# Kernel optimization log

Measured on AMD Instinct MI355X. Metric: run time of the kernel, lower is better.

The kernel has to match this reference:

```python
import jax, jax.numpy as jnp
import numpy as np

N_NODES = 50000
N_EDGES = 1600000
N_FEATURES = 1433
HIDDEN = 256
N_CLASSES = 7


def setup_inputs() -> dict:
    key = jax.random.key(0)
    ks = jax.random.split(key, 5)
    x = jax.random.normal(ks[0], (N_NODES, N_FEATURES), dtype=jnp.float32)
    edge_index = jax.random.randint(ks[1], (2, N_EDGES), 0, N_NODES, dtype=jnp.int64)
    # Glorot-style init like PyG's Linear inside GCNConv
    W1 = jax.random.normal(ks[2], (N_FEATURES, HIDDEN), dtype=jnp.float32) * (1.0 / np.sqrt(N_FEATURES))
    b1 = jnp.zeros((HIDDEN,), dtype=jnp.float32)
    W2 = jax.random.normal(ks[3], (HIDDEN, N_CLASSES), dtype=jnp.float32) * (1.0 / np.sqrt(HIDDEN))
    b2 = jnp.zeros((N_CLASSES,), dtype=jnp.float32)
    return {"x": x, "edge_index": edge_index, "W1": W1, "b1": b1, "W2": W2, "b2": b2}


def _gcn_conv(x, W, b, src, dst, n_nodes):
    """PyG GCNConv: add self-loops, symmetric deg^{-1/2} norm, linear, scatter-add, +bias."""
    h = x @ W  # [N, out]
    loop = jnp.arange(n_nodes, dtype=src.dtype)
    src2 = jnp.concatenate([src, loop])
    dst2 = jnp.concatenate([dst, loop])
    ones = jnp.ones(src2.shape[0], dtype=h.dtype)
    deg = jax.ops.segment_sum(ones, dst2, num_segments=n_nodes)
    dinv = jnp.where(deg > 0, jax.lax.rsqrt(deg), 0.0)
    norm = dinv[src2] * dinv[dst2]  # [E+N]
    msg = h[src2] * norm[:, None]   # gather + scale
    out = jax.ops.segment_sum(msg, dst2, num_segments=n_nodes)
    return out + b


def reference(x, edge_index, W1, b1, W2, b2):
    src, dst = edge_index[0], edge_index[1]
    h = _gcn_conv(x, W1, b1, src, dst, N_NODES)
    h = jax.nn.relu(h)
    # dropout p=0.5 is identity in eval mode (training=False)
    out = _gcn_conv(h, W2, b2, src, dst, N_NODES)
    return out
```

## Files before the change

kernel.cpp:

```cpp
#include <hip/hip_runtime.h>
#include <hip/hip_bf16.h>


#define N_NODES_   50000
#define NB_ROWS_   50048
#define N_EDGES_   1600000
#define N_FEAT_    1433
#define K_PAD_     1440
#define HIDDEN_    256
#define N_CLASSES_ 7

typedef __attribute__((ext_vector_type(8))) short short8;
typedef __attribute__((ext_vector_type(4))) float f32x4;
typedef unsigned int u32;
typedef unsigned short u16;

__device__ __forceinline__ u16 f2bf(float f) {
    __hip_bfloat16 h = __float2bfloat16(f);
    return *(u16*)&h;
}
__device__ __forceinline__ float bf2f(u16 u) {
    return __uint_as_float((u32)u << 16);
}
__device__ __forceinline__ void global_to_lds16(const void* g, void* l) {
    __builtin_amdgcn_global_load_lds(
        (const __attribute__((address_space(1))) u32*)g,
        (__attribute__((address_space(3))) u32*)l, 16, 0, 0);
}

__global__ void deg_kernel(const int* __restrict__ dst, int* __restrict__ deg) {
    int i = blockIdx.x * blockDim.x + threadIdx.x;
    if (i < N_EDGES_) atomicAdd(&deg[dst[i]], 1);
}

__global__ void dinv_kernel(const int* __restrict__ deg, float* __restrict__ dinv) {
    int i = blockIdx.x * blockDim.x + threadIdx.x;
    if (i < N_NODES_) dinv[i] = rsqrtf((float)(deg[i] + 1));
}

#define SCAN_T 256
#define CHUNK_ ((N_NODES_ + SCAN_T - 1) / SCAN_T)
__global__ __launch_bounds__(SCAN_T) void scan_kernel(const int* __restrict__ deg,
                                                      int* __restrict__ row_ptr,
                                                      int* __restrict__ cursor) {
    __shared__ int sums[SCAN_T];
    int t = threadIdx.x;
    int lo = t * CHUNK_, hi = min(lo + CHUNK_, N_NODES_);
    int s = 0;
    for (int i = lo; i < hi; i++) s += deg[i];
    sums[t] = s;
    __syncthreads();
    for (int off = 1; off < SCAN_T; off <<= 1) {
        int v = (t >= off) ? sums[t - off] : 0;
        __syncthreads();
        sums[t] += v;
        __syncthreads();
    }
    int run = (t == 0) ? 0 : sums[t - 1];
    for (int i = lo; i < hi; i++) {
        row_ptr[i] = run;
        cursor[i]  = run;
        run += deg[i];
    }
    if (t == SCAN_T - 1) row_ptr[N_NODES_] = run;
}

__global__ void csr_scatter_kernel(const int* __restrict__ src, const int* __restrict__ dst,
                                   int* __restrict__ cursor, int* __restrict__ csr_src) {
    int i = blockIdx.x * blockDim.x + threadIdx.x;
    if (i >= N_EDGES_) return;
    int d = dst[i];
    int pos = atomicAdd(&cursor[d], 1);
    csr_src[pos] = src[i];
}

__global__ __launch_bounds__(256) void cvt_kernel(const float* __restrict__ x,
                                                  u16* __restrict__ xb) {
    int row = blockIdx.x;
    int t = threadIdx.x;
    const float* xr = x + (long)row * N_FEAT_;
    u16* xbr = xb + (long)row * K_PAD_;
    bool valid = row < N_NODES_;
    for (int k = t; k < K_PAD_; k += 256) {
        float v = (valid && k < N_FEAT_) ? xr[k] : 0.f;
        xbr[k] = f2bf(v);
    }
}

__global__ void w1t_kernel(const float* __restrict__ W1, u16* __restrict__ W1T) {
    int gid = blockIdx.x * blockDim.x + threadIdx.x;
    if (gid >= HIDDEN_ * K_PAD_) return;
    int k = gid % K_PAD_, n = gid / K_PAD_;
    float v = (k < N_FEAT_) ? W1[(long)k * HIDDEN_ + n] : 0.f;
    W1T[(long)n * K_PAD_ + k] = f2bf(v);
}

#define BM 128
#define BN 128
#define BK 32
__global__ __launch_bounds__(256) void gemm1_mfma(const u16* __restrict__ A,
                                                  const u16* __restrict__ BT,
                                                  u16* __restrict__ C) {
    __shared__ u16 As[BM * BK];
    __shared__ u16 Bs[BN * BK];

    const int tid  = threadIdx.x;
    const int lane = tid & 63;
    const int wv   = tid >> 6;
    const int row0 = blockIdx.x * BM;
    const int col0 = blockIdx.y * BN;
    const int wr0  = (wv >> 1) * 64;
    const int wc0  = (wv & 1) * 64;

    f32x4 acc[4][4] = {};

    const int srow = lane >> 2;
    const int skk  = (lane & 3) * 8;

    for (int k0 = 0; k0 < K_PAD_; k0 += BK) {
        #pragma unroll
        for (int j = 0; j < 2; j++) {
            int rbase = wv * 32 + j * 16;
            const u16* g = A + (long)(row0 + rbase + srow) * K_PAD_ + k0 + skk;
            global_to_lds16(g, &As[rbase * BK]);
        }
        #pragma unroll
        for (int j = 0; j < 2; j++) {
            int rbase = j * 64 + wv * 16;
            const u16* g = BT + (long)(col0 + rbase + srow) * K_PAD_ + k0 + skk;
            global_to_lds16(g, &Bs[rbase * BK]);
        }
        __syncthreads();

        const int fm = lane & 15;
        const int fq = (lane >> 4) * 8;
        short8 af[4], bf[4];
        #pragma unroll
        for (int mi = 0; mi < 4; mi++)
            af[mi] = *(const short8*)&As[(wr0 + mi * 16 + fm) * BK + fq];
        #pragma unroll
        for (int ni = 0; ni < 4; ni++)
            bf[ni] = *(const short8*)&Bs[(wc0 + ni * 16 + fm) * BK + fq];
        #pragma unroll
        for (int mi = 0; mi < 4; mi++)
            #pragma unroll
            for (int ni = 0; ni < 4; ni++)
                acc[mi][ni] = __builtin_amdgcn_mfma_f32_16x16x32_bf16(af[mi], bf[ni], acc[mi][ni], 0, 0, 0);
        __syncthreads();
    }

    const int fm = lane & 15;
    const int q4 = (lane >> 4) * 4;
    #pragma unroll
    for (int mi = 0; mi < 4; mi++) {
        #pragma unroll
        for (int r = 0; r < 4; r++) {
            int gm = row0 + wr0 + mi * 16 + q4 + r;
            if (gm < N_NODES_) {
                #pragma unroll
                for (int ni = 0; ni < 4; ni++) {
                    int gn = col0 + wc0 + ni * 16 + fm;
                    C[(long)gm * HIDDEN_ + gn] = f2bf(acc[mi][ni][r]);
                }
            }
        }
    }
}

__global__ __launch_bounds__(256) void agg_gemm2_kernel(const u16* __restrict__ h1b,
                                                        const int* __restrict__ row_ptr,
                                                        const int* __restrict__ csr_src,
                                                        const float* __restrict__ dinv,
                                                        const float* __restrict__ b1,
                                                        const float* __restrict__ W2,
                                                        float* __restrict__ h2) {
    __shared__ float w2s[HIDDEN_ * N_CLASSES_];
    __shared__ float b1s[HIDDEN_];
    int tid = threadIdx.x;
    for (int i = tid; i < HIDDEN_ * N_CLASSES_; i += 256) w2s[i] = W2[i];
    for (int i = tid; i < HIDDEN_; i += 256) b1s[i] = b1[i];
    __syncthreads();

    int wave = tid >> 6;
    int lane = tid & 63;
    int node = blockIdx.x * 4 + wave;
    if (node >= N_NODES_) return;

    int e0 = row_ptr[node], e1 = row_ptr[node + 1];
    float ax = 0.f, ay = 0.f, az = 0.f, aw = 0.f;
    for (int base = e0; base < e1; base += 64) {
        int myE = base + lane;
        int sL = 0;
        float nsL = 0.f;
        if (myE < e1) {
            sL = csr_src[myE];
            nsL = dinv[sL];
        }
        int cnt4 = (min(64, e1 - base) + 3) & ~3;
        for (int j = 0; j < cnt4; j += 4) {
            #pragma unroll
            for (int t = 0; t < 4; t++) {
                int s   = __shfl(sL, j + t, 64);
                float ns = __shfl(nsL, j + t, 64);
                ushort4 u = ((const ushort4*)(h1b + (long)s * HIDDEN_))[lane];
                ax += bf2f(u.x) * ns;
                ay += bf2f(u.y) * ns;
                az += bf2f(u.z) * ns;
                aw += bf2f(u.w) * ns;
            }
        }
    }
    float nd = dinv[node];
    ushort4 su = ((const ushort4*)(h1b + (long)node * HIDDEN_))[lane];
    float xv[4];
    xv[0] = fmaxf(ax * nd + bf2f(su.x) * nd * nd + b1s[lane * 4 + 0], 0.f);
    xv[1] = fmaxf(ay * nd + bf2f(su.y) * nd * nd + b1s[lane * 4 + 1], 0.f);
    xv[2] = fmaxf(az * nd + bf2f(su.z) * nd * nd + b1s[lane * 4 + 2], 0.f);
    xv[3] = fmaxf(aw * nd + bf2f(su.w) * nd * nd + b1s[lane * 4 + 3], 0.f);

    float p[N_CLASSES_];
    #pragma unroll
    for (int c = 0; c < N_CLASSES_; c++) {
        float a = 0.f;
        #pragma unroll
        for (int i = 0; i < 4; i++)
            a += xv[i] * w2s[(lane * 4 + i) * N_CLASSES_ + c];
        p[c] = a;
    }
    #pragma unroll
    for (int off = 32; off > 0; off >>= 1)
        #pragma unroll
        for (int c = 0; c < N_CLASSES_; c++)
            p[c] += __shfl_down(p[c], off, 64);
    if (lane == 0) {
        #pragma unroll
        for (int c = 0; c < N_CLASSES_; c++)
            h2[(long)node * N_CLASSES_ + c] = p[c];
    }
}

__global__ void out_kernel(const float* __restrict__ h2,
                           const int* __restrict__ row_ptr,
                           const int* __restrict__ csr_src,
                           const float* __restrict__ dinv,
                           const float* __restrict__ b2,
                           float* __restrict__ out) {
    long gid = (long)blockIdx.x * blockDim.x + threadIdx.x;
    int node = (int)(gid >> 3);
    int c = (int)(gid & 7);
    if (node >= N_NODES_ || c >= N_CLASSES_) return;
    int e0 = row_ptr[node], e1 = row_ptr[node + 1];
    float acc = 0.f;
    for (int e = e0; e < e1; e++) {
        int s = csr_src[e];
        acc += h2[(long)s * N_CLASSES_ + c] * dinv[s];
    }
    float nd = dinv[node];
    out[(long)node * N_CLASSES_ + c] =
        acc * nd + h2[(long)node * N_CLASSES_ + c] * nd * nd + b2[c];
}

extern "C" void kernel_launch(void* const* d_in, const int* in_sizes, int n_in,
                              void* d_out, int out_size, void* d_ws, size_t ws_size,
                              hipStream_t stream) {
    const float* x   = (const float*)d_in[0];
    const int*   ei  = (const int*)d_in[1];
    const int*   src = ei;
    const int*   dst = ei + N_EDGES_;
    const float* W1  = (const float*)d_in[2];
    const float* b1  = (const float*)d_in[3];
    const float* W2  = (const float*)d_in[4];
    const float* b2  = (const float*)d_in[5];
    float* out = (float*)d_out;

    char* ws = (char*)d_ws;
    size_t off = 0;
    auto alloc = [&](size_t bytes) { void* p = ws + off; off = (off + bytes + 255) & ~(size_t)255; return p; };
    u16*   xb      = (u16*)alloc((size_t)NB_ROWS_ * K_PAD_ * 2);
    u16*   h1b     = (u16*)alloc((size_t)N_NODES_ * HIDDEN_ * 2);
    u16*   w1t     = (u16*)alloc((size_t)HIDDEN_ * K_PAD_ * 2);
    float* h2      = (float*)alloc((size_t)N_NODES_ * N_CLASSES_ * 4);
    int*   deg     = (int*)alloc((size_t)N_NODES_ * 4);
    float* dinv    = (float*)alloc((size_t)N_NODES_ * 4);
    int*   row_ptr = (int*)alloc((size_t)(N_NODES_ + 1) * 4);
    int*   cursor  = (int*)alloc((size_t)N_NODES_ * 4);
    int*   csr_src = (int*)alloc((size_t)N_EDGES_ * 4);

    hipMemsetAsync(deg, 0, (size_t)N_NODES_ * 4, stream);

    deg_kernel<<<(N_EDGES_ + 255) / 256, 256, 0, stream>>>(dst, deg);
    dinv_kernel<<<(N_NODES_ + 255) / 256, 256, 0, stream>>>(deg, dinv);
    scan_kernel<<<1, SCAN_T, 0, stream>>>(deg, row_ptr, cursor);
    csr_scatter_kernel<<<(N_EDGES_ + 255) / 256, 256, 0, stream>>>(src, dst, cursor, csr_src);

    cvt_kernel<<<NB_ROWS_, 256, 0, stream>>>(x, xb);
    w1t_kernel<<<(HIDDEN_ * K_PAD_ + 255) / 256, 256, 0, stream>>>(W1, w1t);

    gemm1_mfma<<<dim3(NB_ROWS_ / BM, HIDDEN_ / BN), 256, 0, stream>>>(xb, w1t, h1b);

    agg_gemm2_kernel<<<(N_NODES_ + 3) / 4, 256, 0, stream>>>(h1b, row_ptr, csr_src, dinv, b1, W2, h2);

    long out_threads = (long)N_NODES_ * 8;
    out_kernel<<<(unsigned)((out_threads + 255) / 256), 256, 0, stream>>>(h2, row_ptr, csr_src, dinv, b2, out);
}
```

Baseline: 964.3 us.

## Prescale features by source dinv, parallelize CSR scan, vectorize conversion and gathers

Folds the source-side deg^-1/2 factor into the GEMM1 epilogue and the layer-2 projection, so the gather loops no longer load dinv per edge. Zero-padded sentinel rows let unrolled gathers skip bounds handling. The single-block scan becomes a three-kernel multi-block scan, the bf16 conversion writes 8-wide vectors, and the next edge-index batch is prefetched in aggregation. This adds extra launches and memsets and changes the h2 row stride to 8.

After: 893.8 us. 1.08x faster.

```diff
diff --git a/kernel.cpp b/kernel.cpp
--- a/kernel.cpp
+++ b/kernel.cpp
@@ -9,8 +9,10 @@
 #define K_PAD_     1440
 #define HIDDEN_    256
 #define N_CLASSES_ 7
+#define NPART_     ((N_NODES_ + 255) / 256)
 
 typedef __attribute__((ext_vector_type(8))) short short8;
+typedef __attribute__((ext_vector_type(8))) unsigned short ushort8;
 typedef __attribute__((ext_vector_type(4))) float f32x4;
 typedef unsigned int u32;
 typedef unsigned short u16;
@@ -38,31 +40,59 @@
     if (i < N_NODES_) dinv[i] = rsqrtf((float)(deg[i] + 1));
 }
 
-#define SCAN_T 256
-#define CHUNK_ ((N_NODES_ + SCAN_T - 1) / SCAN_T)
-__global__ __launch_bounds__(SCAN_T) void scan_kernel(const int* __restrict__ deg,
-                                                      int* __restrict__ row_ptr,
-                                                      int* __restrict__ cursor) {
-    __shared__ int sums[SCAN_T];
+__global__ __launch_bounds__(256) void scan1_kernel(const int* __restrict__ deg,
+                                                    int* __restrict__ partial) {
+    __shared__ int ws[4];
+    int t = threadIdx.x, b = blockIdx.x;
+    int idx = b * 256 + t;
+    int v = (idx < N_NODES_) ? deg[idx] : 0;
+    #pragma unroll
+    for (int off = 32; off > 0; off >>= 1) v += __shfl_down(v, off, 64);
+    if ((t & 63) == 0) ws[t >> 6] = v;
+    __syncthreads();
+    if (t == 0) partial[b] = ws[0] + ws[1] + ws[2] + ws[3];
+}
+
+__global__ __launch_bounds__(256) void scan2_kernel(int* __restrict__ partial,
+                                                    int* __restrict__ blk_off) {
+    __shared__ int sh[256];
     int t = threadIdx.x;
-    int lo = t * CHUNK_, hi = min(lo + CHUNK_, N_NODES_);
-    int s = 0;
-    for (int i = lo; i < hi; i++) s += deg[i];
-    sums[t] = s;
+    int v = (t < NPART_) ? partial[t] : 0;
+    sh[t] = v;
     __syncthreads();
-    for (int off = 1; off < SCAN_T; off <<= 1) {
-        int v = (t >= off) ? sums[t - off] : 0;
-        __syncthreads();
-        sums[t] += v;
-        __syncthreads();
-    }
-    int run = (t == 0) ? 0 : sums[t - 1];
-    for (int i = lo; i < hi; i++) {
-        row_ptr[i] = run;
-        cursor[i]  = run;
-        run += deg[i];
-    }
-    if (t == SCAN_T - 1) row_ptr[N_NODES_] = run;
+    #pragma unroll
+    for (int off = 1; off < 256; off <<= 1) {
+        int a = (t >= off) ? sh[t - off] : 0;
+        __syncthreads();
+        sh[t] += a;
+        __syncthreads();
+    }
+    if (t < NPART_) blk_off[t] = sh[t] - v;
+}
+
+__global__ __launch_bounds__(256) void scan3_kernel(const int* __restrict__ deg,
+                                                    const int* __restrict__ blk_off,
+                                                    int* __restrict__ row_ptr,
+                                                    int* __restrict__ cursor) {
+    __shared__ int sh[256];
+    int t = threadIdx.x, b = blockIdx.x;
+    int idx = b * 256 + t;
+    int v = (idx < N_NODES_) ? deg[idx] : 0;
+    sh[t] = v;
+    __syncthreads();
+    #pragma unroll
+    for (int off = 1; off < 256; off <<= 1) {
+        int a = (t >= off) ? sh[t - off] : 0;
+        __syncthreads();
+        sh[t] += a;
+        __syncthreads();
+    }
+    if (idx < N_NODES_) {
+        int rp = blk_off[b] + sh[t] - v;
+        row_ptr[idx] = rp;
+        cursor[idx]  = rp;
+    }
+    if (idx == 0) row_ptr[N_NODES_] = N_EDGES_;
 }
 
 __global__ void csr_scatter_kernel(const int* __restrict__ src, const int* __restrict__ dst,
@@ -74,17 +104,22 @@
     csr_src[pos] = src[i];
 }
 
-__global__ __launch_bounds__(256) void cvt_kernel(const float* __restrict__ x,
+__global__ __launch_bounds__(192) void cvt_kernel(const float* __restrict__ x,
                                                   u16* __restrict__ xb) {
     int row = blockIdx.x;
     int t = threadIdx.x;
+    if (t >= K_PAD_ / 8) return;
+    int k0 = t * 8;
     const float* xr = x + (long)row * N_FEAT_;
-    u16* xbr = xb + (long)row * K_PAD_;
-    bool valid = row < N_NODES_;
-    for (int k = t; k < K_PAD_; k += 256) {
-        float v = (valid && k < N_FEAT_) ? xr[k] : 0.f;
-        xbr[k] = f2bf(v);
-    }
+    bool vrow = row < N_NODES_;
+    ushort8 o;
+    #pragma unroll
+    for (int j = 0; j < 8; j++) {
+        int k = k0 + j;
+        float v = (vrow && k < N_FEAT_) ? xr[k] : 0.f;
+        o[j] = f2bf(v);
+    }
+    *(ushort8*)(xb + (long)row * K_PAD_ + k0) = o;
 }
 
 __global__ void w1t_kernel(const float* __restrict__ W1, u16* __restrict__ W1T) {
@@ -100,6 +135,7 @@
 #define BK 32
 __global__ __launch_bounds__(256) void gemm1_mfma(const u16* __restrict__ A,
                                                   const u16* __restrict__ BT,
+                                                  const float* __restrict__ dinv,
                                                   u16* __restrict__ C) {
     __shared__ u16 As[BM * BK];
     __shared__ u16 Bs[BN * BK];
@@ -157,23 +193,24 @@
         for (int r = 0; r < 4; r++) {
             int gm = row0 + wr0 + mi * 16 + q4 + r;
             if (gm < N_NODES_) {
+                float sc = dinv[gm];
                 #pragma unroll
                 for (int ni = 0; ni < 4; ni++) {
                     int gn = col0 + wc0 + ni * 16 + fm;
-                    C[(long)gm * HIDDEN_ + gn] = f2bf(acc[mi][ni][r]);
+                    C[(long)gm * HIDDEN_ + gn] = f2bf(acc[mi][ni][r] * sc);
                 }
             }
         }
     }
 }
 
-__global__ __launch_bounds__(256) void agg_gemm2_kernel(const u16* __restrict__ h1b,
+__global__ __launch_bounds__(256) void agg_gemm2_kernel(const u16* __restrict__ h1s,
                                                         const int* __restrict__ row_ptr,
                                                         const int* __restrict__ csr_src,
                                                         const float* __restrict__ dinv,
                                                         const float* __restrict__ b1,
                                                         const float* __restrict__ W2,
-                                                        float* __restrict__ h2) {
+                                                        float* __restrict__ h2s) {
     __shared__ float w2s[HIDDEN_ * N_CLASSES_];
     __shared__ float b1s[HIDDEN_];
     int tid = threadIdx.x;
@@ -188,35 +225,32 @@
 
     int e0 = row_ptr[node], e1 = row_ptr[node + 1];
     float ax = 0.f, ay = 0.f, az = 0.f, aw = 0.f;
+
+    int sL = (e0 + lane < e1) ? csr_src[e0 + lane] : N_NODES_;
     for (int base = e0; base < e1; base += 64) {
-        int myE = base + lane;
-        int sL = 0;
-        float nsL = 0.f;
-        if (myE < e1) {
-            sL = csr_src[myE];
-            nsL = dinv[sL];
-        }
-        int cnt4 = (min(64, e1 - base) + 3) & ~3;
-        for (int j = 0; j < cnt4; j += 4) {
+        int sCur = sL;
+        int nb = base + 64;
+        if (nb < e1) sL = (nb + lane < e1) ? csr_src[nb + lane] : N_NODES_;
+        int cnt8 = (min(64, e1 - base) + 7) & ~7;
+        for (int j = 0; j < cnt8; j += 8) {
             #pragma unroll
-            for (int t = 0; t < 4; t++) {
-                int s   = __shfl(sL, j + t, 64);
-                float ns = __shfl(nsL, j + t, 64);
-                ushort4 u = ((const ushort4*)(h1b + (long)s * HIDDEN_))[lane];
-                ax += bf2f(u.x) * ns;
-                ay += bf2f(u.y) * ns;
-                az += bf2f(u.z) * ns;
-                aw += bf2f(u.w) * ns;
+            for (int t = 0; t < 8; t++) {
+                int s = __shfl(sCur, j + t, 64);
+                ushort4 u = ((const ushort4*)(h1s + (long)s * HIDDEN_))[lane];
+                ax += bf2f(u.x);
+                ay += bf2f(u.y);
+                az += bf2f(u.z);
+                aw += bf2f(u.w);
             }
         }
     }
     float nd = dinv[node];
-    ushort4 su = ((const ushort4*)(h1b + (long)node * HIDDEN_))[lane];
+    ushort4 su = ((const ushort4*)(h1s + (long)node * HIDDEN_))[lane];
     float xv[4];
-    xv[0] = fmaxf(ax * nd + bf2f(su.x) * nd * nd + b1s[lane * 4 + 0], 0.f);
-    xv[1] = fmaxf(ay * nd + bf2f(su.y) * nd * nd + b1s[lane * 4 + 1], 0.f);
-    xv[2] = fmaxf(az * nd + bf2f(su.z) * nd * nd + b1s[lane * 4 + 2], 0.f);
-    xv[3] = fmaxf(aw * nd + bf2f(su.w) * nd * nd + b1s[lane * 4 + 3], 0.f);
+    xv[0] = fmaxf((ax + bf2f(su.x)) * nd + b1s[lane * 4 + 0], 0.f);
+    xv[1] = fmaxf((ay + bf2f(su.y)) * nd + b1s[lane * 4 + 1], 0.f);
+    xv[2] = fmaxf((az + bf2f(su.z)) * nd + b1s[lane * 4 + 2], 0.f);
+    xv[3] = fmaxf((aw + bf2f(su.w)) * nd + b1s[lane * 4 + 3], 0.f);
 
     float p[N_CLASSES_];
     #pragma unroll
@@ -235,11 +269,11 @@
     if (lane == 0) {
         #pragma unroll
         for (int c = 0; c < N_CLASSES_; c++)
-            h2[(long)node * N_CLASSES_ + c] = p[c];
-    }
-}
-
-__global__ void out_kernel(const float* __restrict__ h2,
+            h2s[(long)node * 8 + c] = p[c] * nd;
+    }
+}
+
+__global__ void out_kernel(const float* __restrict__ h2s,
                            const int* __restrict__ row_ptr,
                            const int* __restrict__ csr_src,
                            const float* __restrict__ dinv,
@@ -251,13 +285,20 @@
     if (node >= N_NODES_ || c >= N_CLASSES_) return;
     int e0 = row_ptr[node], e1 = row_ptr[node + 1];
     float acc = 0.f;
-    for (int e = e0; e < e1; e++) {
-        int s = csr_src[e];
-        acc += h2[(long)s * N_CLASSES_ + c] * dinv[s];
+    for (int e = e0; e < e1; e += 4) {
+        int s0 = csr_src[e];
+        int s1 = (e + 1 < e1) ? csr_src[e + 1] : N_NODES_;
+        int s2 = (e + 2 < e1) ? csr_src[e + 2] : N_NODES_;
+        int s3 = (e + 3 < e1) ? csr_src[e + 3] : N_NODES_;
+        float v0 = h2s[(long)s0 * 8 + c];
+        float v1 = h2s[(long)s1 * 8 + c];
+        float v2 = h2s[(long)s2 * 8 + c];
+        float v3 = h2s[(long)s3 * 8 + c];
+        acc += (v0 + v1) + (v2 + v3);
     }
     float nd = dinv[node];
     out[(long)node * N_CLASSES_ + c] =
-        acc * nd + h2[(long)node * N_CLASSES_ + c] * nd * nd + b2[c];
+        (acc + h2s[(long)node * 8 + c]) * nd + b2[c];
 }
 
 extern "C" void kernel_launch(void* const* d_in, const int* in_sizes, int n_in,
@@ -277,29 +318,35 @@
     size_t off = 0;
     auto alloc = [&](size_t bytes) { void* p = ws + off; off = (off + bytes + 255) & ~(size_t)255; return p; };
     u16*   xb      = (u16*)alloc((size_t)NB_ROWS_ * K_PAD_ * 2);
-    u16*   h1b     = (u16*)alloc((size_t)N_NODES_ * HIDDEN_ * 2);
+    u16*   h1s     = (u16*)alloc((size_t)(N_NODES_ + 1) * HIDDEN_ * 2);
     u16*   w1t     = (u16*)alloc((size_t)HIDDEN_ * K_PAD_ * 2);
-    float* h2      = (float*)alloc((size_t)N_NODES_ * N_CLASSES_ * 4);
+    float* h2s     = (float*)alloc((size_t)(N_NODES_ + 1) * 8 * 4);
     int*   deg     = (int*)alloc((size_t)N_NODES_ * 4);
     float* dinv    = (float*)alloc((size_t)N_NODES_ * 4);
     int*   row_ptr = (int*)alloc((size_t)(N_NODES_ + 1) * 4);
     int*   cursor  = (int*)alloc((size_t)N_NODES_ * 4);
     int*   csr_src = (int*)alloc((size_t)N_EDGES_ * 4);
+    int*   partial = (int*)alloc((size_t)NPART_ * 4);
+    int*   blk_off = (int*)alloc((size_t)NPART_ * 4);
 
     hipMemsetAsync(deg, 0, (size_t)N_NODES_ * 4, stream);
+    hipMemsetAsync(h1s + (size_t)N_NODES_ * HIDDEN_, 0, HIDDEN_ * 2, stream);
+    hipMemsetAsync(h2s + (size_t)N_NODES_ * 8, 0, 8 * 4, stream);
 
     deg_kernel<<<(N_EDGES_ + 255) / 256, 256, 0, stream>>>(dst, deg);
     dinv_kernel<<<(N_NODES_ + 255) / 256, 256, 0, stream>>>(deg, dinv);
-    scan_kernel<<<1, SCAN_T, 0, stream>>>(deg, row_ptr, cursor);
+    scan1_kernel<<<NPART_, 256, 0, stream>>>(deg, partial);
+    scan2_kernel<<<1, 256, 0, stream>>>(partial, blk_off);
+    scan3_kernel<<<NPART_, 256, 0, stream>>>(deg, blk_off, row_ptr, cursor);
     csr_scatter_kernel<<<(N_EDGES_ + 255) / 256, 256, 0, stream>>>(src, dst, cursor, csr_src);
 
-    cvt_kernel<<<NB_ROWS_, 256, 0, stream>>>(x, xb);
+    cvt_kernel<<<NB_ROWS_, 192, 0, stream>>>(x, xb);
     w1t_kernel<<<(HIDDEN_ * K_PAD_ + 255) / 256, 256, 0, stream>>>(W1, w1t);
 
-    gemm1_mfma<<<dim3(NB_ROWS_ / BM, HIDDEN_ / BN), 256, 0, stream>>>(xb, w1t, h1b);
-
-    agg_gemm2_kernel<<<(N_NODES_ + 3) / 4, 256, 0, stream>>>(h1b, row_ptr, csr_src, dinv, b1, W2, h2);
+    gemm1_mfma<<<dim3(NB_ROWS_ / BM, HIDDEN_ / BN), 256, 0, stream>>>(xb, w1t, dinv, h1s);
+
+    agg_gemm2_kernel<<<(N_NODES_ + 3) / 4, 256, 0, stream>>>(h1s, row_ptr, csr_src, dinv, b1, W2, h2s);
 
     long out_threads = (long)N_NODES_ * 8;
-    out_kernel<<<(unsigned)((out_threads + 255) / 256), 256, 0, stream>>>(h2, row_ptr, csr_src, dinv, b2, out);
-}
+    out_kernel<<<(unsigned)((out_threads + 255) / 256), 256, 0, stream>>>(h2s, row_ptr, csr_src, dinv, b2, out);
+}
```
